# Kernel optimization log

Hardware: AMD Instinct MI355X
Metric: run time of the kernel (lower is better)

The kernel has to match this reference:

```python
import jax, jax.numpy as jnp
import numpy as np

# Hyperparameters matching the torch module instantiation
STRIDE = (2, 2, 2)
PADDING = (1, 1, 1)
OUTPUT_PADDING = (1, 1, 1)
DILATION = (2, 2, 2)
KERNEL = (3, 3, 3)


def setup_inputs() -> dict:
    key = jax.random.key(0)
    k1, k2, k3 = jax.random.split(key, 3)
    x = jax.random.normal(k1, (2, 64, 32, 32, 32), dtype=jnp.float32)
    # torch ConvTranspose3d weight layout: (C_in, C_out//groups, kD, kH, kW)
    weight = jax.random.normal(k2, (64, 32, 3, 3, 3), dtype=jnp.float32) * 0.05
    bias = jax.random.normal(k3, (32,), dtype=jnp.float32) * 0.05
    return {"x": x, "weight": weight, "bias": bias}


def reference(x, weight, bias):
    # Same math as the naive torch module: zero-insertion upsample by stride,
    # symmetric pad by dilation*(k-1)-padding, dense conv3d with the spatially
    # flipped weight at rhs dilation, trailing output_padding, then bias add.
    # lhs_dilation performs the zero-insertion implicitly (identical result).
    pad = tuple(max(0, d * (k - 1) - p)
                for d, k, p in zip(DILATION, KERNEL, PADDING))
    # (C_in, C_out, k,k,k) -> (C_out, C_in, k,k,k), flipped spatially
    w = jnp.flip(jnp.transpose(weight, (1, 0, 2, 3, 4)), axis=(2, 3, 4))
    out = jax.lax.conv_general_dilated(
        x, w,
        window_strides=(1, 1, 1),
        padding=[(p, p) for p in pad],
        lhs_dilation=STRIDE,
        rhs_dilation=DILATION,
        dimension_numbers=("NCDHW", "OIDHW", "NCDHW"),
    )
    opd, oph, opw = OUTPUT_PADDING
    out = jnp.pad(out, ((0, 0), (0, 0), (0, opd), (0, oph), (0, opw)))
    return out + bias[None, :, None, None, None]
```

## Files before the change

### kernel.cpp

```cpp
#include <hip/hip_runtime.h>


#define DOUT 66
#define PL (DOUT*DOUT)
#define ROW_B 4352

typedef _Float16 half8   __attribute__((ext_vector_type(8)));
typedef float    floatx16 __attribute__((ext_vector_type(16)));
typedef float    floatx4  __attribute__((ext_vector_type(4)));
typedef float    floatx2  __attribute__((ext_vector_type(2)));

__global__ void __launch_bounds__(256) wprep(const float* __restrict__ w,
                                             _Float16* __restrict__ wA)
{
    int o = blockIdx.x * 256 + threadIdx.x;
    int j = o & 7;
    int tmp = o >> 3;
    int lane = tmp & 63;
    int g = tmp >> 6;
    int cc = g / 27, tap = g - cc * 27;
    int co = lane & 31, khalf = lane >> 5;
    int ci = cc * 16 + khalf * 8 + j;
    wA[o] = (_Float16)w[ci * 864 + co * 27 + tap];
}

__global__ void __launch_bounds__(256, 3) convt(
    const float* __restrict__ x, const _Float16* __restrict__ wA,
    const float* __restrict__ bias, float* __restrict__ out)
{
    __shared__ __align__(16) unsigned char xlds[52224];

    const int tid  = threadIdx.x;
    const int lane = tid & 63;
    const int wv   = tid >> 6;

    unsigned b = blockIdx.x;
    const unsigned xcd = b & 7u;
    const int n   = (int)(xcd & 1u);
    const unsigned rest = b >> 3;
    const int dp  = (int)(rest & 31u);
    const int hq2 = (int)(rest >> 5);
    const int hpg = (int)((xcd >> 1) * 4 + hq2);
    const int hpb = hpg * 2;

    const float* xn = x + (size_t)n * 2097152;
    const int gq  = tid & 7;
    const int ccg = (tid >> 3) & 7;
    #pragma unroll
    for (int k = 0; k < 3; ++k) {
        const int r  = k * 4 + wv;
        const int id = dp  - 1 + (r >> 2);
        const int ih = hpb - 1 + (r & 3);
        unsigned char* dst = xlds + r * ROW_B + ccg * 544 + (gq * 4 + 1) * 16;
        if (((unsigned)id < 32u) & ((unsigned)ih < 32u)) {
            const float* src = xn + ccg * 262144 + (id * 32 + ih) * 32 + gq * 4;
            floatx4 f0 = *(const floatx4*)(src);
            floatx4 f1 = *(const floatx4*)(src + 32768);
            floatx4 f2 = *(const floatx4*)(src + 2 * 32768);
            floatx4 f3 = *(const floatx4*)(src + 3 * 32768);
            floatx4 f4 = *(const floatx4*)(src + 4 * 32768);
            floatx4 f5 = *(const floatx4*)(src + 5 * 32768);
            floatx4 f6 = *(const floatx4*)(src + 6 * 32768);
            floatx4 f7 = *(const floatx4*)(src + 7 * 32768);
            #pragma unroll
            for (int m = 0; m < 4; ++m) {
                unsigned p0 = __builtin_bit_cast(unsigned,
                    __builtin_amdgcn_cvt_pkrtz(f0[m], f1[m]));
                unsigned p1 = __builtin_bit_cast(unsigned,
                    __builtin_amdgcn_cvt_pkrtz(f2[m], f3[m]));
                unsigned p2 = __builtin_bit_cast(unsigned,
                    __builtin_amdgcn_cvt_pkrtz(f4[m], f5[m]));
                unsigned p3 = __builtin_bit_cast(unsigned,
                    __builtin_amdgcn_cvt_pkrtz(f6[m], f7[m]));
                *(uint4*)(dst + m * 16) = make_uint4(p0, p1, p2, p3);
            }
        } else {
            #pragma unroll
            for (int m = 0; m < 4; ++m)
                *(uint4*)(dst + m * 16) = make_uint4(0, 0, 0, 0);
        }
    }
    if (tid < 192) {
        const int r   = tid >> 4;
        const int rem = tid & 15;
        const int cg  = rem >> 1, side = rem & 1;
        *(uint4*)(xlds + r * ROW_B + cg * 544 + (side ? 33 * 16 : 0)) =
            make_uint4(0, 0, 0, 0);
    }

    uint4 A[27];
    const _Float16* wl = wA + ((size_t)wv * 27 * 64 + lane) * 8;
    #pragma unroll
    for (int t = 0; t < 27; ++t) A[t] = *(const uint4*)(wl + t * 512);

    __syncthreads();

    const int wp    = lane & 31;
    const int khalf = lane >> 5;
    const int cbase = (2 * wv + khalf) * 544 + wp * 16;

    floatx16 acc0 = {}, acc1 = {};
    #pragma unroll
    for (int kd = 0; kd < 3; ++kd)
    #pragma unroll
    for (int kh = 0; kh < 3; ++kh)
    #pragma unroll
    for (int kw = 0; kw < 3; ++kw) {
        const int tap  = (kd * 3 + kh) * 3 + kw;
        const int row0 = (2 - kd) * 4 + (2 - kh);
        const uint4* bp0 = (const uint4*)(xlds + row0 * ROW_B + cbase + (2 - kw) * 16);
        acc0 = __builtin_amdgcn_mfma_f32_32x32x16_f16(
            __builtin_bit_cast(half8, A[tap]),
            __builtin_bit_cast(half8, bp0[0]), acc0, 0, 0, 0);
        const uint4* bp1 = (const uint4*)((const char*)bp0 + ROW_B);
        acc1 = __builtin_amdgcn_mfma_f32_32x32x16_f16(
            __builtin_bit_cast(half8, A[tap]),
            __builtin_bit_cast(half8, bp1[0]), acc1, 0, 0, 0);
    }

    __syncthreads();
    float* part = (float*)xlds;
    if (wv != 0) {
        #pragma unroll
        for (int r = 0; r < 16; ++r)
            part[((wv * 2 + 0) * 16 + r) * 64 + lane] = acc0[r];
    }
    if (wv != 1) {
        #pragma unroll
        for (int r = 0; r < 16; ++r)
            part[((wv * 2 + 1) * 16 + r) * 64 + lane] = acc1[r];
    }
    __syncthreads();

    const int od = 2 * dp + 1;
    if (wv <= 1) {
        float s[16];
        #pragma unroll
        for (int r = 0; r < 16; ++r) {
            s[r] = (wv == 0) ? acc0[r] : acc1[r];
            #pragma unroll
            for (int w2 = 0; w2 < 4; ++w2) {
                if (w2 == wv) continue;
                s[r] += part[((w2 * 2 + wv) * 16 + r) * 64 + lane];
            }
        }
        const int oh = 2 * (hpb + wv) + 1;
        #pragma unroll
        for (int r = 0; r < 16; ++r) {
            const int co = (r & 3) + 8 * (r >> 2) + 4 * khalf;
            const float bv = bias[co];
            floatx2* orow = (floatx2*)(out +
                ((size_t)(n * 32 + co) * DOUT + od) * PL + oh * DOUT);
            floatx2 vv = {bv, s[r] + bv};
            __builtin_nontemporal_store(vv, orow + wp);
            if (wp == 31) {
                floatx2 bb2 = {bv, bv};
                __builtin_nontemporal_store(bb2, orow + 32);
            }
        }
    } else {
        const bool tails = (hpg == 15);
        const bool extra = (dp == 31);
        const int ohA = (wv == 2) ? 2 * hpb : 2 * hpb + 2;
        const int ohT = (wv == 2) ? 64 : 65;
        const int e0  = 4 * hpg + ((wv == 2) ? 0 : 2);
        auto putrow = [&](float* plane, int oh, floatx2 bb) {
            floatx2* rw = (floatx2*)(plane + oh * DOUT);
            __builtin_nontemporal_store(bb, rw + wp);
            if (wp == 31) __builtin_nontemporal_store(bb, rw + 32);
        };
        #pragma unroll
        for (int r = 0; r < 16; ++r) {
            const int co = (r & 3) + 8 * (r >> 2) + 4 * khalf;
            const float bv = bias[co];
            const floatx2 bb = {bv, bv};
            float* pc    = out + (size_t)(n * 32 + co) * ((size_t)DOUT * PL);
            float* podd  = pc + (size_t)od * PL;
            float* peven = pc + (size_t)(od - 1) * PL;
            putrow(podd, ohA, bb);
            if (tails) putrow(podd, ohT, bb);
            putrow(peven, e0, bb);
            putrow(peven, e0 + 1, bb);
            if (tails) putrow(peven, ohT, bb);
            if (extra) {
                float* p64 = pc + (size_t)64 * PL;
                float* p65 = pc + (size_t)65 * PL;
                putrow(p64, e0, bb);
                putrow(p64, e0 + 1, bb);
                putrow(p65, e0, bb);
                putrow(p65, e0 + 1, bb);
                if (tails) {
                    putrow(p64, ohT, bb);
                    putrow(p65, ohT, bb);
                }
            }
        }
    }
}

extern "C" void kernel_launch(void* const* d_in, const int* in_sizes, int n_in,
                              void* d_out, int out_size, void* d_ws, size_t ws_size,
                              hipStream_t stream) {
    const float* x    = (const float*)d_in[0];
    const float* wgt  = (const float*)d_in[1];
    const float* bias = (const float*)d_in[2];
    float* out = (float*)d_out;
    _Float16* wA = (_Float16*)d_ws;

    wprep<<<216, 256, 0, stream>>>(wgt, wA);
    convt<<<1024, 256, 0, stream>>>(x, wA, bias, out);
}
```

Before: 125.0 us.

## Process two depth planes per block, reusing staged input slabs with prefetch

Each block now computes two consecutive output depth planes instead of one. It stages three input depth slices once and prefetches the fourth into a separate LDS slot while the first plane's MFMAs run. This cuts redundant global loads and fp16 conversion of overlapping input slices and halves the grid. The cross-wave reduction is resequenced to reuse a single slot-sized LDS buffer, and bias is loaded once into registers. The cost is more LDS per block, a lower occupancy target of two blocks per unit, and fewer blocks to spread across the GPU.

```diff
diff --git a/kernel.cpp b/kernel.cpp
--- a/kernel.cpp
+++ b/kernel.cpp
@@ -4,6 +4,7 @@
 #define DOUT 66
 #define PL (DOUT*DOUT)
 #define ROW_B 4352
+#define SLOT_B 17408
 
 typedef _Float16 half8   __attribute__((ext_vector_type(8)));
 typedef float    floatx16 __attribute__((ext_vector_type(16)));
@@ -24,11 +25,11 @@
     wA[o] = (_Float16)w[ci * 864 + co * 27 + tap];
 }
 
-__global__ void __launch_bounds__(256, 3) convt(
+__global__ void __launch_bounds__(256, 2) convt(
     const float* __restrict__ x, const _Float16* __restrict__ wA,
     const float* __restrict__ bias, float* __restrict__ out)
 {
-    __shared__ __align__(16) unsigned char xlds[52224];
+    __shared__ __align__(16) unsigned char xlds[4 * SLOT_B];
 
     const int tid  = threadIdx.x;
     const int lane = tid & 63;
@@ -38,40 +39,37 @@
     const unsigned xcd = b & 7u;
     const int n   = (int)(xcd & 1u);
     const unsigned rest = b >> 3;
-    const int dp  = (int)(rest & 31u);
-    const int hq2 = (int)(rest >> 5);
+    const int hq2   = (int)(rest & 3u);
+    const int dpair = (int)(rest >> 2);
     const int hpg = (int)((xcd >> 1) * 4 + hq2);
     const int hpb = hpg * 2;
+    const int dp0 = dpair * 2;
 
     const float* xn = x + (size_t)n * 2097152;
     const int gq  = tid & 7;
     const int ccg = (tid >> 3) & 7;
-    #pragma unroll
-    for (int k = 0; k < 3; ++k) {
-        const int r  = k * 4 + wv;
-        const int id = dp  - 1 + (r >> 2);
-        const int ih = hpb - 1 + (r & 3);
-        unsigned char* dst = xlds + r * ROW_B + ccg * 544 + (gq * 4 + 1) * 16;
-        if (((unsigned)id < 32u) & ((unsigned)ih < 32u)) {
+    const int ihl = wv;
+    const int ih  = hpb - 1 + ihl;
+    const bool ihok = (unsigned)ih < 32u;
+
+    auto stage = [&](int slot, int id) {
+        unsigned char* dst = xlds + slot * SLOT_B + ihl * ROW_B
+                           + ccg * 544 + (gq * 4 + 1) * 16;
+        if (ihok & ((unsigned)id < 32u)) {
             const float* src = xn + ccg * 262144 + (id * 32 + ih) * 32 + gq * 4;
-            floatx4 f0 = *(const floatx4*)(src);
-            floatx4 f1 = *(const floatx4*)(src + 32768);
-            floatx4 f2 = *(const floatx4*)(src + 2 * 32768);
-            floatx4 f3 = *(const floatx4*)(src + 3 * 32768);
-            floatx4 f4 = *(const floatx4*)(src + 4 * 32768);
-            floatx4 f5 = *(const floatx4*)(src + 5 * 32768);
-            floatx4 f6 = *(const floatx4*)(src + 6 * 32768);
-            floatx4 f7 = *(const floatx4*)(src + 7 * 32768);
+            floatx4 f[8];
+            #pragma unroll
+            for (int j = 0; j < 8; ++j) f[j] = *(const floatx4*)(src + j * 32768);
             #pragma unroll
             for (int m = 0; m < 4; ++m) {
                 unsigned p0 = __builtin_bit_cast(unsigned,
-                    __builtin_amdgcn_cvt_pkrtz(f0[m], f1[m]));
+                    __builtin_amdgcn_cvt_pkrtz(f[0][m], f[1][m]));
                 unsigned p1 = __builtin_bit_cast(unsigned,
-                    __builtin_amdgcn_cvt_pkrtz(f2[m], f3[m]));
+                    __builtin_amdgcn_cvt_pkrtz(f[2][m], f[3][m]));
                 unsigned p2 = __builtin_bit_cast(unsigned,
-                    __builtin_amdgcn_cvt_pkrtz(f4[m], f5[m]));
+                    __builtin_amdgcn_cvt_pkrtz(f[4][m], f[5][m]));
                 unsigned p3 = __builtin_bit_cast(unsigned,
-                    __builtin_amdgcn_cvt_pkrtz(f6[m], f7[m]));
+                    __builtin_amdgcn_cvt_pkrtz(f[6][m], f[7][m]));
                 *(uint4*)(dst + m * 16) = make_uint4(p0, p1, p2, p3);
             }
         } else {
@@ -79,122 +77,202 @@
             for (int m = 0; m < 4; ++m)
                 *(uint4*)(dst + m * 16) = make_uint4(0, 0, 0, 0);
         }
-    }
-    if (tid < 192) {
-        const int r   = tid >> 4;
-        const int rem = tid & 15;
-        const int cg  = rem >> 1, side = rem & 1;
-        *(uint4*)(xlds + r * ROW_B + cg * 544 + (side ? 33 * 16 : 0)) =
-            make_uint4(0, 0, 0, 0);
-    }
+        if (tid < 64) {
+            const int r2 = tid >> 4, rem = tid & 15;
+            const int cg = rem >> 1, side = rem & 1;
+            *(uint4*)(xlds + slot * SLOT_B + r2 * ROW_B + cg * 544
+                      + (side ? 33 * 16 : 0)) = make_uint4(0, 0, 0, 0);
+        }
+    };
+
+    floatx4 pf[8];
+    bool pfv = false;
+    auto pf_load = [&](int id) {
+        pfv = ihok & ((unsigned)id < 32u);
+        if (pfv) {
+            const float* src = xn + ccg * 262144 + (id * 32 + ih) * 32 + gq * 4;
+            #pragma unroll
+            for (int j = 0; j < 8; ++j) pf[j] = *(const floatx4*)(src + j * 32768);
+        }
+    };
+    auto pf_write = [&](int slot) {
+        unsigned char* dst = xlds + slot * SLOT_B + ihl * ROW_B
+                           + ccg * 544 + (gq * 4 + 1) * 16;
+        if (pfv) {
+            #pragma unroll
+            for (int m = 0; m < 4; ++m) {
+                unsigned p0 = __builtin_bit_cast(unsigned,
+                    __builtin_amdgcn_cvt_pkrtz(pf[0][m], pf[1][m]));
+                unsigned p1 = __builtin_bit_cast(unsigned,
+                    __builtin_amdgcn_cvt_pkrtz(pf[2][m], pf[3][m]));
+                unsigned p2 = __builtin_bit_cast(unsigned,
+                    __builtin_amdgcn_cvt_pkrtz(pf[4][m], pf[5][m]));
+                unsigned p3 = __builtin_bit_cast(unsigned,
+                    __builtin_amdgcn_cvt_pkrtz(pf[6][m], pf[7][m]));
+                *(uint4*)(dst + m * 16) = make_uint4(p0, p1, p2, p3);
+            }
+        } else {
+            #pragma unroll
+            for (int m = 0; m < 4; ++m)
+                *(uint4*)(dst + m * 16) = make_uint4(0, 0, 0, 0);
+        }
+        if (tid < 64) {
+            const int r2 = tid >> 4, rem = tid & 15;
+            const int cg = rem >> 1, side = rem & 1;
+            *(uint4*)(xlds + slot * SLOT_B + r2 * ROW_B + cg * 544
+                      + (side ? 33 * 16 : 0)) = make_uint4(0, 0, 0, 0);
+        }
+    };
 
     uint4 A[27];
     const _Float16* wl = wA + ((size_t)wv * 27 * 64 + lane) * 8;
     #pragma unroll
     for (int t = 0; t < 27; ++t) A[t] = *(const uint4*)(wl + t * 512);
 
-    __syncthreads();
-
     const int wp    = lane & 31;
     const int khalf = lane >> 5;
     const int cbase = (2 * wv + khalf) * 544 + wp * 16;
 
-    floatx16 acc0 = {}, acc1 = {};
+    float bv[16];
     #pragma unroll
-    for (int kd = 0; kd < 3; ++kd)
-    #pragma unroll
-    for (int kh = 0; kh < 3; ++kh)
-    #pragma unroll
-    for (int kw = 0; kw < 3; ++kw) {
-        const int tap  = (kd * 3 + kh) * 3 + kw;
-        const int row0 = (2 - kd) * 4 + (2 - kh);
-        const uint4* bp0 = (const uint4*)(xlds + row0 * ROW_B + cbase + (2 - kw) * 16);
-        acc0 = __builtin_amdgcn_mfma_f32_32x32x16_f16(
-            __builtin_bit_cast(half8, A[tap]),
-            __builtin_bit_cast(half8, bp0[0]), acc0, 0, 0, 0);
-        const uint4* bp1 = (const uint4*)((const char*)bp0 + ROW_B);
-        acc1 = __builtin_amdgcn_mfma_f32_32x32x16_f16(
-            __builtin_bit_cast(half8, A[tap]),
-            __builtin_bit_cast(half8, bp1[0]), acc1, 0, 0, 0);
+    for (int r = 0; r < 16; ++r)
+        bv[r] = bias[(r & 3) + 8 * (r >> 2) + 4 * khalf];
+
+    stage(0, dp0 - 1);
+    stage(1, dp0);
+    stage(2, dp0 + 1);
+    __syncthreads();
+
+    auto mfma_unit = [&](int base, floatx16& a0, floatx16& a1) {
+        #pragma unroll
+        for (int kd = 0; kd < 3; ++kd)
+        #pragma unroll
+        for (int kh = 0; kh < 3; ++kh)
+        #pragma unroll
+        for (int kw = 0; kw < 3; ++kw) {
+            const int tap = (kd * 3 + kh) * 3 + kw;
+            const uint4* bp0 = (const uint4*)(xlds + (base + 2 - kd) * SLOT_B
+                               + (2 - kh) * ROW_B + cbase + (2 - kw) * 16);
+            a0 = __builtin_amdgcn_mfma_f32_32x32x16_f16(
+                __builtin_bit_cast(half8, A[tap]),
+                __builtin_bit_cast(half8, bp0[0]), a0, 0, 0, 0);
+            const uint4* bp1 = (const uint4*)((const char*)bp0 + ROW_B);
+            acc1_step:
+            a1 = __builtin_amdgcn_mfma_f32_32x32x16_f16(
+                __builtin_bit_cast(half8, A[tap]),
+                __builtin_bit_cast(half8, bp1[0]), a1, 0, 0, 0);
+        }
+    };
+
+    auto reduce_store = [&](int u, int dp, floatx16& a0, floatx16& a1) {
+        float* part = (float*)(xlds + u * SLOT_B);
+        const int od = 2 * dp + 1;
+
+        __syncthreads();
+        if (wv != 0) {
+            #pragma unroll
+            for (int r = 0; r < 16; ++r)
+                part[(wv - 1) * 1024 + r * 64 + lane] = a0[r];
+        }
+        __syncthreads();
+        float s[16];
+        if (wv == 0) {
+            #pragma unroll
+            for (int r = 0; r < 16; ++r)
+                s[r] = a0[r] + part[r * 64 + lane]
+                             + part[1024 + r * 64 + lane]
+                             + part[2048 + r * 64 + lane];
+        }
+        __syncthreads();
+        if (wv != 1) {
+            const int idx = (wv == 0) ? 0 : (wv - 1);
+            #pragma unroll
+            for (int r = 0; r < 16; ++r)
+                part[idx * 1024 + r * 64 + lane] = a1[r];
+        }
+        if (wv == 0) {
+            const int oh = 2 * hpb + 1;
+            #pragma unroll
+            for (int r = 0; r < 16; ++r) {
+                const int co = (r & 3) + 8 * (r >> 2) + 4 * khalf;
+                floatx2* orow = (floatx2*)(out +
+                    ((size_t)(n * 32 + co) * DOUT + od) * PL + oh * DOUT);
+                floatx2 vv = {bv[r], s[r] + bv[r]};
+                __builtin_nontemporal_store(vv, orow + wp);
+                if (wp == 31) {
+                    floatx2 bb = {bv[r], bv[r]};
+                    __builtin_nontemporal_store(bb, orow + 32);
+                }
+            }
+        }
+        __syncthreads();
+        if (wv == 1) {
+            float s1[16];
+            #pragma unroll
+            for (int r = 0; r < 16; ++r)
+                s1[r] = a1[r] + part[r * 64 + lane]
+                              + part[1024 + r * 64 + lane]
+                              + part[2048 + r * 64 + lane];
+            const int oh = 2 * hpb + 3;
+            #pragma unroll
+            for (int r = 0; r < 16; ++r) {
+                const int co = (r & 3) + 8 * (r >> 2) + 4 * khalf;
+                floatx2* orow = (floatx2*)(out +
+                    ((size_t)(n * 32 + co) * DOUT + od) * PL + oh * DOUT);
+                floatx2 vv = {bv[r], s1[r] + bv[r]};
+                __builtin_nontemporal_store(vv, orow + wp);
+                if (wp == 31) {
+                    floatx2 bb = {bv[r], bv[r]};
+                    __builtin_nontemporal_store(bb, orow + 32);
+                }
+            }
+        } else if (wv >= 2) {
+            const bool tails = (hpg == 15);
+            const bool extra = (dp == 31);
+            const int ohA = (wv == 2) ? 2 * hpb : 2 * hpb + 2;
+            const int ohT = (wv == 2) ? 64 : 65;
+            const int e0  = 4 * hpg + ((wv == 2) ? 0 : 2);
+            auto putrow = [&](float* plane, int oh, floatx2 bb) {
+                floatx2* rw = (floatx2*)(plane + oh * DOUT);
+                __builtin_nontemporal_store(bb, rw + wp);
+                if (wp == 31) __builtin_nontemporal_store(bb, rw + 32);
+            };
+            #pragma unroll
+            for (int r = 0; r < 16; ++r) {
+                const int co = (r & 3) + 8 * (r >> 2) + 4 * khalf;
+                const floatx2 bb = {bv[r], bv[r]};
+                float* pc    = out + (size_t)(n * 32 + co) * ((size_t)DOUT * PL);
+                float* podd  = pc + (size_t)od * PL;
+                float* peven = pc + (size_t)(od - 1) * PL;
+                putrow(podd, ohA, bb);
+                if (tails) putrow(podd, ohT, bb);
+                putrow(peven, e0, bb);
+                putrow(peven, e0 + 1, bb);
+                if (tails) putrow(peven, ohT, bb);
+                if (extra) {
+                    float* p64 = pc + (size_t)64 * PL;
+                    float* p65 = pc + (size_t)65 * PL;
+                    putrow(p64, e0, bb);
+                    putrow(p64, e0 + 1, bb);
+                    putrow(p65, e0, bb);
+                    putrow(p65, e0 + 1, bb);
+                    if (tails) { putrow(p64, ohT, bb); putrow(p65, ohT, bb); }
+                }
+            }
+        }
+    };
+
+    {
+        floatx16 a0 = {}, a1 = {};
+        pf_load(dp0 + 2);
+        mfma_unit(0, a0, a1);
+        pf_write(3);
+        reduce_store(0, dp0, a0, a1);
     }
-
-    __syncthreads();
-    float* part = (float*)xlds;
-    if (wv != 0) {
-        #pragma unroll
-        for (int r = 0; r < 16; ++r)
-            part[((wv * 2 + 0) * 16 + r) * 64 + lane] = acc0[r];
-    }
-    if (wv != 1) {
-        #pragma unroll
-        for (int r = 0; r < 16; ++r)
-            part[((wv * 2 + 1) * 16 + r) * 64 + lane] = acc1[r];
-    }
-    __syncthreads();
-
-    const int od = 2 * dp + 1;
-    if (wv <= 1) {
-        float s[16];
-        #pragma unroll
-        for (int r = 0; r < 16; ++r) {
-            s[r] = (wv == 0) ? acc0[r] : acc1[r];
-            #pragma unroll
-            for (int w2 = 0; w2 < 4; ++w2) {
-                if (w2 == wv) continue;
-                s[r] += part[((w2 * 2 + wv) * 16 + r) * 64 + lane];
-            }
-        }
-        const int oh = 2 * (hpb + wv) + 1;
-        #pragma unroll
-        for (int r = 0; r < 16; ++r) {
-            const int co = (r & 3) + 8 * (r >> 2) + 4 * khalf;
-            const float bv = bias[co];
-            floatx2* orow = (floatx2*)(out +
-                ((size_t)(n * 32 + co) * DOUT + od) * PL + oh * DOUT);
-            floatx2 vv = {bv, s[r] + bv};
-            __builtin_nontemporal_store(vv, orow + wp);
-            if (wp == 31) {
-                floatx2 bb2 = {bv, bv};
-                __builtin_nontemporal_store(bb2, orow + 32);
-            }
-        }
-    } else {
-        const bool tails = (hpg == 15);
-        const bool extra = (dp == 31);
-        const int ohA = (wv == 2) ? 2 * hpb : 2 * hpb + 2;
-        const int ohT = (wv == 2) ? 64 : 65;
-        const int e0  = 4 * hpg + ((wv == 2) ? 0 : 2);
-        auto putrow = [&](float* plane, int oh, floatx2 bb) {
-            floatx2* rw = (floatx2*)(plane + oh * DOUT);
-            __builtin_nontemporal_store(bb, rw + wp);
-            if (wp == 31) __builtin_nontemporal_store(bb, rw + 32);
-        };
-        #pragma unroll
-        for (int r = 0; r < 16; ++r) {
-            const int co = (r & 3) + 8 * (r >> 2) + 4 * khalf;
-            const float bv = bias[co];
-            const floatx2 bb = {bv, bv};
-            float* pc    = out + (size_t)(n * 32 + co) * ((size_t)DOUT * PL);
-            float* podd  = pc + (size_t)od * PL;
-            float* peven = pc + (size_t)(od - 1) * PL;
-            putrow(podd, ohA, bb);
-            if (tails) putrow(podd, ohT, bb);
-            putrow(peven, e0, bb);
-            putrow(peven, e0 + 1, bb);
-            if (tails) putrow(peven, ohT, bb);
-            if (extra) {
-                float* p64 = pc + (size_t)64 * PL;
-                float* p65 = pc + (size_t)65 * PL;
-                putrow(p64, e0, bb);
-                putrow(p64, e0 + 1, bb);
-                putrow(p65, e0, bb);
-                putrow(p65, e0 + 1, bb);
-                if (tails) {
-                    putrow(p64, ohT, bb);
-                    putrow(p65, ohT, bb);
-                }
-            }
-        }
+    {
+        floatx16 a0 = {}, a1 = {};
+        mfma_unit(1, a0, a1);
+        reduce_store(1, dp0 + 1, a0, a1);
     }
 }
 
@@ -208,5 +286,5 @@
     _Float16* wA = (_Float16*)d_ws;
 
     wprep<<<216, 256, 0, stream>>>(wgt, wA);
-    convt<<<1024, 256, 0, stream>>>(x, wA, bias, out);
+    convt<<<512, 256, 0, stream>>>(x, wA, bias, out);
 }
```

Result: no change. 126.2 us (+0.9%).

## Restructure convT blocks to four output rows with contiguous float4 output stores

Applied to the files above, without the earlier changes.

Each block now covers four input h-rows instead of two, halving the grid, and each wave owns one output row and loops over all four channel chunks. This removes the cross-wave partial-sum reduction through LDS. Results are staged in LDS so that each thread writes whole contiguous 66-wide output row segments as float4 stores, replacing the scattered float2 nontemporal stores and separate bias-row writes. The cost is a larger LDS footprint (occupancy bound lowered to 2), reloading weights per chunk inside the MFMA loop, and per-element index arithmetic in the store loop.

```diff
diff --git a/kernel.cpp b/kernel.cpp
--- a/kernel.cpp
+++ b/kernel.cpp
@@ -4,11 +4,11 @@
 #define DOUT 66
 #define PL (DOUT*DOUT)
 #define ROW_B 4352
+#define IDG_B (6*ROW_B)
 
 typedef _Float16 half8   __attribute__((ext_vector_type(8)));
 typedef float    floatx16 __attribute__((ext_vector_type(16)));
 typedef float    floatx4  __attribute__((ext_vector_type(4)));
-typedef float    floatx2  __attribute__((ext_vector_type(2)));
 
 __global__ void __launch_bounds__(256) wprep(const float* __restrict__ w,
                                              _Float16* __restrict__ wA)
@@ -24,11 +24,11 @@
     wA[o] = (_Float16)w[ci * 864 + co * 27 + tap];
 }
 
-__global__ void __launch_bounds__(256, 3) convt(
+__global__ void __launch_bounds__(256, 2) convt(
     const float* __restrict__ x, const _Float16* __restrict__ wA,
     const float* __restrict__ bias, float* __restrict__ out)
 {
-    __shared__ __align__(16) unsigned char xlds[52224];
+    __shared__ __align__(16) unsigned char xlds[3 * IDG_B];
 
     const int tid  = threadIdx.x;
     const int lane = tid & 63;
@@ -36,163 +36,135 @@
 
     unsigned b = blockIdx.x;
     const unsigned xcd = b & 7u;
-    const int n   = (int)(xcd & 1u);
+    const int n     = (int)(xcd & 1u);
     const unsigned rest = b >> 3;
-    const int dp  = (int)(rest & 31u);
-    const int hq2 = (int)(rest >> 5);
-    const int hpg = (int)((xcd >> 1) * 4 + hq2);
-    const int hpb = hpg * 2;
+    const int hpg   = (int)((xcd >> 1) * 2 + (rest & 1u));
+    const int dp    = (int)(rest >> 1);
+    const int hpb   = hpg * 4;
 
     const float* xn = x + (size_t)n * 2097152;
-    const int gq  = tid & 7;
-    const int ccg = (tid >> 3) & 7;
-    #pragma unroll
-    for (int k = 0; k < 3; ++k) {
-        const int r  = k * 4 + wv;
-        const int id = dp  - 1 + (r >> 2);
-        const int ih = hpb - 1 + (r & 3);
-        unsigned char* dst = xlds + r * ROW_B + ccg * 544 + (gq * 4 + 1) * 16;
-        if (((unsigned)id < 32u) & ((unsigned)ih < 32u)) {
-            const float* src = xn + ccg * 262144 + (id * 32 + ih) * 32 + gq * 4;
-            floatx4 f0 = *(const floatx4*)(src);
-            floatx4 f1 = *(const floatx4*)(src + 32768);
-            floatx4 f2 = *(const floatx4*)(src + 2 * 32768);
-            floatx4 f3 = *(const floatx4*)(src + 3 * 32768);
-            floatx4 f4 = *(const floatx4*)(src + 4 * 32768);
-            floatx4 f5 = *(const floatx4*)(src + 5 * 32768);
-            floatx4 f6 = *(const floatx4*)(src + 6 * 32768);
-            floatx4 f7 = *(const floatx4*)(src + 7 * 32768);
-            #pragma unroll
-            for (int m = 0; m < 4; ++m) {
-                unsigned p0 = __builtin_bit_cast(unsigned,
-                    __builtin_amdgcn_cvt_pkrtz(f0[m], f1[m]));
-                unsigned p1 = __builtin_bit_cast(unsigned,
-                    __builtin_amdgcn_cvt_pkrtz(f2[m], f3[m]));
-                unsigned p2 = __builtin_bit_cast(unsigned,
-                    __builtin_amdgcn_cvt_pkrtz(f4[m], f5[m]));
-                unsigned p3 = __builtin_bit_cast(unsigned,
-                    __builtin_amdgcn_cvt_pkrtz(f6[m], f7[m]));
-                *(uint4*)(dst + m * 16) = make_uint4(p0, p1, p2, p3);
+
+    const int co_s = tid >> 3;
+    const int l8   = tid & 7;
+    const float bvc = bias[co_s];
+    const floatx4 bb4 = {bvc, bvc, bvc, bvc};
+
+    {
+        for (int t = tid; t < 1152; t += 256) {
+            const int r   = t >> 6;
+            const int ccg = (t >> 3) & 7;
+            const int gq  = t & 7;
+            const int id_l = r / 6, ihl = r - 6 * id_l;
+            const int id = dp - 1 + id_l;
+            const int ih = hpb - 1 + ihl;
+            unsigned char* dst = xlds + (id_l * 6 + ihl) * ROW_B
+                               + ccg * 544 + (gq * 4 + 1) * 16;
+            if (((unsigned)id < 32u) & ((unsigned)ih < 32u)) {
+                const float* src = xn + ccg * 262144 + (id * 32 + ih) * 32 + gq * 4;
+                floatx4 f[8];
+                #pragma unroll
+                for (int j = 0; j < 8; ++j) f[j] = *(const floatx4*)(src + j * 32768);
+                #pragma unroll
+                for (int m = 0; m < 4; ++m) {
+                    unsigned p0 = __builtin_bit_cast(unsigned,
+                        __builtin_amdgcn_cvt_pkrtz(f[0][m], f[1][m]));
+                    unsigned p1 = __builtin_bit_cast(unsigned,
+                        __builtin_amdgcn_cvt_pkrtz(f[2][m], f[3][m]));
+                    unsigned p2 = __builtin_bit_cast(unsigned,
+                        __builtin_amdgcn_cvt_pkrtz(f[4][m], f[5][m]));
+                    unsigned p3 = __builtin_bit_cast(unsigned,
+                        __builtin_amdgcn_cvt_pkrtz(f[6][m], f[7][m]));
+                    *(uint4*)(dst + m * 16) = make_uint4(p0, p1, p2, p3);
+                }
+            } else {
+                #pragma unroll
+                for (int m = 0; m < 4; ++m)
+                    *(uint4*)(dst + m * 16) = make_uint4(0, 0, 0, 0);
             }
-        } else {
-            #pragma unroll
-            for (int m = 0; m < 4; ++m)
-                *(uint4*)(dst + m * 16) = make_uint4(0, 0, 0, 0);
+        }
+        for (int h = tid; h < 288; h += 256) {
+            const int r = h >> 4, rem = h & 15;
+            const int cg = rem >> 1, side = rem & 1;
+            *(uint4*)(xlds + r * ROW_B + cg * 544 + (side ? 33 * 16 : 0)) =
+                make_uint4(0, 0, 0, 0);
         }
     }
-    if (tid < 192) {
-        const int r   = tid >> 4;
-        const int rem = tid & 15;
-        const int cg  = rem >> 1, side = rem & 1;
-        *(uint4*)(xlds + r * ROW_B + cg * 544 + (side ? 33 * 16 : 0)) =
-            make_uint4(0, 0, 0, 0);
+
+    {
+        const int nq = (hpg == 7) ? 165 : 132;
+        float* eb = out + ((size_t)(n * 32 + co_s) * DOUT + 2 * dp) * PL
+                    + 8 * hpg * DOUT;
+        for (int q = l8; q < nq; q += 8) *(floatx4*)(eb + 4 * q) = bb4;
+        if (dp == 31) {
+            float* p64 = out + ((size_t)(n * 32 + co_s) * DOUT + 64) * PL
+                         + 8 * hpg * DOUT;
+            for (int q = l8; q < nq; q += 8) *(floatx4*)(p64 + 4 * q) = bb4;
+            float* p65 = p64 + PL;
+            for (int q = l8; q < nq; q += 8) *(floatx4*)(p65 + 4 * q) = bb4;
+        }
     }
-
-    uint4 A[27];
-    const _Float16* wl = wA + ((size_t)wv * 27 * 64 + lane) * 8;
-    #pragma unroll
-    for (int t = 0; t < 27; ++t) A[t] = *(const uint4*)(wl + t * 512);
-
     __syncthreads();
 
     const int wp    = lane & 31;
     const int khalf = lane >> 5;
-    const int cbase = (2 * wv + khalf) * 544 + wp * 16;
 
-    floatx16 acc0 = {}, acc1 = {};
+    floatx16 acc = {};
     #pragma unroll
-    for (int kd = 0; kd < 3; ++kd)
-    #pragma unroll
-    for (int kh = 0; kh < 3; ++kh)
-    #pragma unroll
-    for (int kw = 0; kw < 3; ++kw) {
-        const int tap  = (kd * 3 + kh) * 3 + kw;
-        const int row0 = (2 - kd) * 4 + (2 - kh);
-        const uint4* bp0 = (const uint4*)(xlds + row0 * ROW_B + cbase + (2 - kw) * 16);
-        acc0 = __builtin_amdgcn_mfma_f32_32x32x16_f16(
-            __builtin_bit_cast(half8, A[tap]),
-            __builtin_bit_cast(half8, bp0[0]), acc0, 0, 0, 0);
-        const uint4* bp1 = (const uint4*)((const char*)bp0 + ROW_B);
-        acc1 = __builtin_amdgcn_mfma_f32_32x32x16_f16(
-            __builtin_bit_cast(half8, A[tap]),
-            __builtin_bit_cast(half8, bp1[0]), acc1, 0, 0, 0);
+    for (int cc = 0; cc < 4; ++cc) {
+        uint4 A[27];
+        const _Float16* wl = wA + ((size_t)cc * 27 * 64 + lane) * 8;
+        #pragma unroll
+        for (int t = 0; t < 27; ++t) A[t] = *(const uint4*)(wl + t * 512);
+        const int cb = (2 * cc + khalf) * 544 + wp * 16;
+        #pragma unroll
+        for (int kd = 0; kd < 3; ++kd)
+        #pragma unroll
+        for (int kh = 0; kh < 3; ++kh)
+        #pragma unroll
+        for (int kw = 0; kw < 3; ++kw) {
+            const int tap = (kd * 3 + kh) * 3 + kw;
+            const uint4* bp = (const uint4*)(xlds
+                + ((2 - kd) * 6 + (wv + 2 - kh)) * ROW_B + cb + (2 - kw) * 16);
+            acc = __builtin_amdgcn_mfma_f32_32x32x16_f16(
+                __builtin_bit_cast(half8, A[tap]),
+                __builtin_bit_cast(half8, bp[0]), acc, 0, 0, 0);
+        }
     }
 
     __syncthreads();
-    float* part = (float*)xlds;
-    if (wv != 0) {
-        #pragma unroll
-        for (int r = 0; r < 16; ++r)
-            part[((wv * 2 + 0) * 16 + r) * 64 + lane] = acc0[r];
-    }
-    if (wv != 1) {
-        #pragma unroll
-        for (int r = 0; r < 16; ++r)
-            part[((wv * 2 + 1) * 16 + r) * 64 + lane] = acc1[r];
+    float* val = (float*)xlds;
+    #pragma unroll
+    for (int r = 0; r < 16; ++r) {
+        const int co = (r & 3) + 8 * (r >> 2) + 4 * khalf;
+        val[((size_t)wv * 32 + co) * 33 + wp] = acc[r];
     }
     __syncthreads();
 
-    const int od = 2 * dp + 1;
-    if (wv <= 1) {
-        float s[16];
+    {
+        float* base = out + ((size_t)(n * 32 + co_s) * DOUT + 2 * dp + 1) * PL
+                      + 8 * hpg * DOUT;
         #pragma unroll
-        for (int r = 0; r < 16; ++r) {
-            s[r] = (wv == 0) ? acc0[r] : acc1[r];
-            #pragma unroll
-            for (int w2 = 0; w2 < 4; ++w2) {
-                if (w2 == wv) continue;
-                s[r] += part[((w2 * 2 + wv) * 16 + r) * 64 + lane];
+        for (int p = 0; p < 17; ++p) {
+            const int q = l8 + 8 * p;
+            if (q < 132) {
+                floatx4 o;
+                #pragma unroll
+                for (int j = 0; j < 4; ++j) {
+                    const int e = 4 * q + j;
+                    const int rl = e / 66;
+                    const int ow = e - rl * 66;
+                    float v = bvc;
+                    if ((rl & 1) && (ow & 1) && ow < 65)
+                        v += val[(((rl >> 1) * 32) + co_s) * 33 + (ow >> 1)];
+                    o[j] = v;
+                }
+                *(floatx4*)(base + 4 * q) = o;
             }
         }
-        const int oh = 2 * (hpb + wv) + 1;
-        #pragma unroll
-        for (int r = 0; r < 16; ++r) {
-            const int co = (r & 3) + 8 * (r >> 2) + 4 * khalf;
-            const float bv = bias[co];
-            floatx2* orow = (floatx2*)(out +
-                ((size_t)(n * 32 + co) * DOUT + od) * PL + oh * DOUT);
-            floatx2 vv = {bv, s[r] + bv};
-            __builtin_nontemporal_store(vv, orow + wp);
-            if (wp == 31) {
-                floatx2 bb2 = {bv, bv};
-                __builtin_nontemporal_store(bb2, orow + 32);
-            }
-        }
-    } else {
-        const bool tails = (hpg == 15);
-        const bool extra = (dp == 31);
-        const int ohA = (wv == 2) ? 2 * hpb : 2 * hpb + 2;
-        const int ohT = (wv == 2) ? 64 : 65;
-        const int e0  = 4 * hpg + ((wv == 2) ? 0 : 2);
-        auto putrow = [&](float* plane, int oh, floatx2 bb) {
-            floatx2* rw = (floatx2*)(plane + oh * DOUT);
-            __builtin_nontemporal_store(bb, rw + wp);
-            if (wp == 31) __builtin_nontemporal_store(bb, rw + 32);
-        };
-        #pragma unroll
-        for (int r = 0; r < 16; ++r) {
-            const int co = (r & 3) + 8 * (r >> 2) + 4 * khalf;
-            const float bv = bias[co];
-            const floatx2 bb = {bv, bv};
-            float* pc    = out + (size_t)(n * 32 + co) * ((size_t)DOUT * PL);
-            float* podd  = pc + (size_t)od * PL;
-            float* peven = pc + (size_t)(od - 1) * PL;
-            putrow(podd, ohA, bb);
-            if (tails) putrow(podd, ohT, bb);
-            putrow(peven, e0, bb);
-            putrow(peven, e0 + 1, bb);
-            if (tails) putrow(peven, ohT, bb);
-            if (extra) {
-                float* p64 = pc + (size_t)64 * PL;
-                float* p65 = pc + (size_t)65 * PL;
-                putrow(p64, e0, bb);
-                putrow(p64, e0 + 1, bb);
-                putrow(p65, e0, bb);
-                putrow(p65, e0 + 1, bb);
-                if (tails) {
-                    putrow(p64, ohT, bb);
-                    putrow(p65, ohT, bb);
-                }
+        if (hpg == 7) {
+            for (int p = 0; p < 5; ++p) {
+                const int q = 132 + l8 + 8 * p;
+                if (q < 165) *(floatx4*)(base + 4 * q) = bb4;
             }
         }
     }
@@ -208,5 +180,5 @@
     _Float16* wA = (_Float16*)d_ws;
 
     wprep<<<216, 256, 0, stream>>>(wgt, wA);
-    convt<<<1024, 256, 0, stream>>>(x, wA, bias, out);
+    convt<<<512, 256, 0, stream>>>(x, wA, bias, out);
 }
```

Result: faster. 105.4 us (-15.7%).
